# Performance work log

Measured on AMD Instinct MI355X. Metric: run time of the kernel, lower is better.

## Reference

```python
import jax, jax.numpy as jnp
import numpy as np

B, T, D, H, K, V, W = 2, 2048, 768, 12, 64, 64, 1024
EPS = 1e-6


def setup_inputs() -> dict:
    key = jax.random.key(0)
    ks = jax.random.split(key, 10)
    std = 0.02
    return {
        "x": jax.random.normal(ks[0], (B, T, D), jnp.float32),
        "gdn_state": jax.random.normal(ks[1], (B, H, K, V), jnp.float32),
        "Wq": jax.random.normal(ks[2], (D, H * K), jnp.float32) * std,
        "Wk": jax.random.normal(ks[3], (D, H * K), jnp.float32) * std,
        "Wv": jax.random.normal(ks[4], (D, H * K), jnp.float32) * std,
        "Wo": jax.random.normal(ks[5], (H * K, D), jnp.float32) * std,
        "Wgq": jax.random.normal(ks[6], (D, H * K), jnp.float32) * std,
        "Wro": jax.random.normal(ks[7], (H * V, D), jnp.float32) * std,
        "Wg": jax.random.normal(ks[8], (D, H), jnp.float32) * std,
        "bg": jnp.full((H,), 1.0, jnp.float32),  # swa_gate_init
        "norm_w": jnp.ones((D,), jnp.float32),
    }


def reference(x, gdn_state, Wq, Wk, Wv, Wo, Wgq, Wro, Wg, bg, norm_w):
    # RMSNorm
    xn = x * jax.lax.rsqrt(jnp.mean(x * x, axis=-1, keepdims=True) + EPS) * norm_w

    def proj(w):  # (B,T,D)@(D,HK) -> (B,H,T,K)
        return (xn @ w).reshape(B, T, H, K).transpose(0, 2, 1, 3)

    q, k, v = proj(Wq), proj(Wk), proj(Wv)
    scale = K ** -0.5

    scores = jnp.einsum("bhqk,bhsk->bhqs", q, k) * scale  # (B,H,T,T)
    i = jnp.arange(T)[:, None]
    j = jnp.arange(T)[None, :]
    allowed = (j <= i) & (j >= i - W)  # causal sliding window
    scores = jnp.where(allowed, scores, -jnp.inf)
    attn = jax.nn.softmax(scores, axis=-1)

    local = jnp.einsum("bhqs,bhsk->bhqk", attn, v)
    local = local.transpose(0, 2, 1, 3).reshape(B, T, H * K) @ Wo  # (B,T,D)

    # GDN state retrieval
    qg = jax.nn.relu((xn @ Wgq).reshape(B, T, H, K).transpose(0, 2, 1, 3))  # (B,H,T,K)
    retrieved = jnp.einsum("bhkv,bhtk->bhtv", gdn_state, qg)  # (B,H,T,V)
    retrieval = retrieved.transpose(0, 2, 1, 3).reshape(B, T, H * V) @ Wro  # (B,T,D)
    gate = jax.nn.sigmoid(xn @ Wg + bg)  # (B,T,H)
    retrieval = jnp.mean(gate, axis=-1, keepdims=True) * retrieval

    return x + local + retrieval
```

## Files before the change

kernel.cpp:

```cpp
#include <hip/hip_runtime.h>
#include <math.h>
#include <stdint.h>

typedef float f32x4 __attribute__((ext_vector_type(4)));
typedef __bf16 bf16x8 __attribute__((ext_vector_type(8)));
typedef __bf16 bf16x4 __attribute__((ext_vector_type(4)));

constexpr int Bc = 2, Tc = 2048, Dc = 768, Hc = 12, Wc = 1024;
#define CEXP 0.18033688011112042f

__device__ __forceinline__ f32x4 mfma_bf16(bf16x8 a, bf16x8 b, f32x4 c) {
    return __builtin_amdgcn_mfma_f32_16x16x32_bf16(a, b, c, 0, 0, 0);
}
__device__ __forceinline__ void gload16(const void* g, void* l) {
    __builtin_amdgcn_global_load_lds(
        (const __attribute__((address_space(1))) uint32_t*)g,
        (__attribute__((address_space(3))) uint32_t*)l, 16, 0, 0);
}
__device__ __forceinline__ uint32_t pack2(float a, float b) {
    union { __bf16 h[2]; uint32_t u; } x;
    x.h[0] = (__bf16)a; x.h[1] = (__bf16)b; return x.u;
}
__device__ __forceinline__ void s_wait_vm4() { asm volatile("s_waitcnt vmcnt(4)" ::: "memory"); }
__device__ __forceinline__ void s_wait_vm2() { asm volatile("s_waitcnt vmcnt(2)" ::: "memory"); }
__device__ __forceinline__ void s_wait_vm0() { asm volatile("s_waitcnt vmcnt(0)" ::: "memory"); }
__device__ __forceinline__ void s_wait_lgkm0() { asm volatile("s_waitcnt lgkmcnt(0)" ::: "memory"); }
__device__ __forceinline__ void bar()        { __builtin_amdgcn_s_barrier(); }
__device__ __forceinline__ void wait_tiles2(int infl) {
    if (infl >= 2) s_wait_vm4();
    else if (infl == 1) s_wait_vm2();
    else s_wait_vm0();
}

__global__ __launch_bounds__(256) void k_prep_w(
    const float* __restrict__ Wq, const float* __restrict__ Wk,
    const float* __restrict__ Wv, const float* __restrict__ Wgq,
    const float* __restrict__ Wo, const float* __restrict__ Wro,
    __bf16* __restrict__ wTproj, __bf16* __restrict__ wTout)
{
    __shared__ __bf16 ldsT[64][66];
    const int wsel = blockIdx.y;
    const float* srcs[6] = {Wq, Wk, Wv, Wgq, Wo, Wro};
    const float* src = srcs[wsel];
    __bf16* dst; int dstride, koff;
    if (wsel < 4) { dst = wTproj + (size_t)wsel * Dc * Dc; dstride = Dc;  koff = 0; }
    else if (wsel == 4) { dst = wTout; dstride = 1536; koff = 0; }
    else { dst = wTout; dstride = 1536; koff = 768; }
    const float scale = (wsel == 0) ? CEXP : 1.0f;

    int tile = blockIdx.x;
    int tk = tile % 12, tn = tile / 12;
    int k0 = tk * 64, n0 = tn * 64;
    int i = threadIdx.x, rsub = i >> 4, c4 = i & 15;
#pragma unroll
    for (int rep = 0; rep < 4; ++rep) {
        int row = rep * 16 + rsub;
        float4 v = *(const float4*)(src + (size_t)(k0 + row) * Dc + n0 + c4 * 4);
        ldsT[c4 * 4 + 0][row] = (__bf16)(v.x * scale);
        ldsT[c4 * 4 + 1][row] = (__bf16)(v.y * scale);
        ldsT[c4 * 4 + 2][row] = (__bf16)(v.z * scale);
        ldsT[c4 * 4 + 3][row] = (__bf16)(v.w * scale);
    }
    __syncthreads();
#pragma unroll
    for (int rep = 0; rep < 4; ++rep) {
        int n = rep * 16 + rsub;
        bf16x4 o = *(const bf16x4*)&ldsT[n][c4 * 4];
        *(bf16x4*)(dst + (size_t)(n0 + n) * dstride + koff + k0 + c4 * 4) = o;
    }
}

__global__ __launch_bounds__(256) void k_prep_state(
    const float* __restrict__ st, __bf16* __restrict__ stT)
{
    int idx = blockIdx.x * 256 + threadIdx.x;
    int bh = idx >> 12, kk = (idx >> 6) & 63, vv = idx & 63;
    stT[(size_t)bh * 4096 + vv * 64 + kk] = (__bf16)st[idx];
}

__global__ __launch_bounds__(256) void k_norm_gate(
    const float* __restrict__ x, const float* __restrict__ norm_w,
    const float* __restrict__ Wg, const float* __restrict__ bg,
    __bf16* __restrict__ xnb, float* __restrict__ gmean)
{
    int row = blockIdx.x, tid = threadIdx.x;
    int wv = tid >> 6;
    const float* xr = x + (size_t)row * Dc;
    float4 v = make_float4(0.f, 0.f, 0.f, 0.f);
    float ss = 0.f;
    if (tid < 192) {
        v = ((const float4*)xr)[tid];
        ss = v.x * v.x + v.y * v.y + v.z * v.z + v.w * v.w;
    }
#pragma unroll
    for (int m = 32; m; m >>= 1) ss += __shfl_xor(ss, m, 64);
    __shared__ float red[4];
    __shared__ float pred[4][12];
    if ((tid & 63) == 0) red[wv] = ss;
    __syncthreads();
    float tot = red[0] + red[1] + red[2] + red[3];
    float rms = rsqrtf(tot * (1.f / 768.f) + 1e-6f);
    float xn0 = 0.f, xn1 = 0.f, xn2 = 0.f, xn3 = 0.f;
    if (tid < 192) {
        float4 nw = ((const float4*)norm_w)[tid];
        xn0 = v.x * rms * nw.x; xn1 = v.y * rms * nw.y;
        xn2 = v.z * rms * nw.z; xn3 = v.w * rms * nw.w;
        bf16x4 o;
        o[0] = (__bf16)xn0; o[1] = (__bf16)xn1; o[2] = (__bf16)xn2; o[3] = (__bf16)xn3;
        *(bf16x4*)(xnb + (size_t)row * Dc + tid * 4) = o;
    }
    float p[12];
#pragma unroll
    for (int h = 0; h < 12; ++h) p[h] = 0.f;
    if (tid < 192) {
        const float* wr = Wg + (size_t)tid * 48;
#pragma unroll
        for (int h = 0; h < 12; ++h)
            p[h] = xn0 * wr[h] + xn1 * wr[12 + h] + xn2 * wr[24 + h] + xn3 * wr[36 + h];
    }
#pragma unroll
    for (int h = 0; h < 12; ++h) {
#pragma unroll
        for (int m = 32; m; m >>= 1) p[h] += __shfl_xor(p[h], m, 64);
    }
    if ((tid & 63) == 0) {
#pragma unroll
        for (int h = 0; h < 12; ++h) pred[wv][h] = p[h];
    }
    __syncthreads();
    if (tid == 0) {
        float s = 0.f;
#pragma unroll
        for (int h = 0; h < 12; ++h) {
            float ph = pred[0][h] + pred[1][h] + pred[2][h] + pred[3][h];
            s += 1.f / (1.f + expf(-(ph + bg[h])));
        }
        gmean[row] = s * (1.f / 12.f);
    }
}

template <int MODE>
__global__ __launch_bounds__(256) void k_gemm(
    const __bf16* __restrict__ A, const __bf16* __restrict__ BT,
    const float* __restrict__ xres, float* __restrict__ outf,
    __bf16* __restrict__ qb, __bf16* __restrict__ kbf,
    __bf16* __restrict__ vtb, __bf16* __restrict__ qgb)
{
    constexpr int BM = (MODE == 0) ? 128 : 64;
    constexpr int BN = (MODE == 0) ? 128 : 64;
    constexpr int KD = (MODE == 0) ? 768 : 1536;
    constexpr int BK = (MODE == 0) ? 32 : 64;
    constexpr int KI = BK / 32;
    constexpr int WM = BM / 2, WN = BN / 2;
    constexpr int MI = WM / 16, NI = WN / 16;
    constexpr int NK = KD / BK;
    constexpr int GR = BK / 8;
    constexpr int ACH = BM * BK / 2048;
    constexpr int BCH = BN * BK / 2048;
    __shared__ __bf16 As[2][BM * BK];
    __shared__ __bf16 Bs[2][BN * BK];
    const int tid = threadIdx.x, w = tid >> 6, lane = tid & 63;
    const int g = lane >> 4, t = lane & 15;
    int id = blockIdx.x, xcd = id & 7, l = id >> 3;
    int m0, n0;
    if (MODE == 0) {
        m0 = (((xcd & 3) * 8) + (l & 7)) * BM;
        n0 = (((xcd >> 2) * 12) + (l >> 3)) * BN;
    } else {
        m0 = ((xcd * 8) + (l & 7)) * BM;
        n0 = (l >> 3) * BN;
    }
    const __bf16* Abase = A + (size_t)m0 * KD;
    const __bf16* Bbase = BT + (size_t)n0 * KD;
    const int wrow = (w >> 1) * WM, wcol = (w & 1) * WN;

    auto STAGE = [&](int buf, int k0) {
#pragma unroll
        for (int c = 0; c < ACH; ++c) {
            int chunk = c * 256 + tid, row = chunk / GR, cix = chunk % GR;
            gload16(Abase + (size_t)row * KD + k0 + cix * 8, &As[buf][chunk * 8]);
        }
#pragma unroll
        for (int c = 0; c < BCH; ++c) {
            int chunk = c * 256 + tid, row = chunk / GR, cix = chunk % GR;
            gload16(Bbase + (size_t)row * KD + k0 + cix * 8, &Bs[buf][chunk * 8]);
        }
    };

    f32x4 acc[MI][NI] = {};
    STAGE(0, 0);
    STAGE(1, BK);
    for (int ks = 0; ks < NK; ++ks) {
        if (ks == NK - 1) s_wait_vm0(); else s_wait_vm4();
        bar();
        const __bf16* Ab = As[ks & 1];
        const __bf16* Bb = Bs[ks & 1];
        bf16x8 af[MI][KI], bfr[NI][KI];
#pragma unroll
        for (int kk = 0; kk < KI; ++kk) {
#pragma unroll
            for (int mi = 0; mi < MI; ++mi)
                af[mi][kk] = *(const bf16x8*)(Ab + (wrow + mi * 16 + t) * BK + kk * 32 + g * 8);
#pragma unroll
            for (int ni = 0; ni < NI; ++ni)
                bfr[ni][kk] = *(const bf16x8*)(Bb + (wcol + ni * 16 + t) * BK + kk * 32 + g * 8);
        }
        s_wait_lgkm0();
        __builtin_amdgcn_sched_barrier(0);
        bar();
        if (ks + 2 < NK) STAGE(ks & 1, (ks + 2) * BK);
        __builtin_amdgcn_s_setprio(1);
#pragma unroll
        for (int kk = 0; kk < KI; ++kk)
#pragma unroll
            for (int mi = 0; mi < MI; ++mi)
#pragma unroll
                for (int ni = 0; ni < NI; ++ni)
                    acc[mi][ni] = mfma_bf16(af[mi][kk], bfr[ni][kk], acc[mi][ni]);
        __builtin_amdgcn_s_setprio(0);
    }
    const int region = (MODE == 0) ? (n0 / 768) : 0;
    if (MODE == 0 && region == 2) {
#pragma unroll
        for (int mi = 0; mi < MI; ++mi)
#pragma unroll
            for (int ni = 0; ni < NI; ++ni) {
                int grow0 = m0 + wrow + mi * 16 + g * 4;
                int b = grow0 >> 11, ti0 = grow0 & (Tc - 1);
                int c = (n0 + wcol + ni * 16 + t) - 1536;
                int h = c >> 6, kd = c & 63;
                int kap = ti0 & 63;
                int rho = (kap & 32) | (((kap >> 2) & 3) << 3) | (((kap >> 4) & 1) << 2);
                int ts = (ti0 & ~63) | (rho ^ ((kd & 7) << 3));
                bf16x4 o;
                o[0] = (__bf16)acc[mi][ni][0]; o[1] = (__bf16)acc[mi][ni][1];
                o[2] = (__bf16)acc[mi][ni][2]; o[3] = (__bf16)acc[mi][ni][3];
                *(bf16x4*)(vtb + ((size_t)(b * Hc + h) * 64 + kd) * Tc + ts) = o;
            }
    } else {
#pragma unroll
        for (int mi = 0; mi < MI; ++mi)
#pragma unroll
            for (int ni = 0; ni < NI; ++ni)
#pragma unroll
                for (int r = 0; r < 4; ++r) {
                    int grow = m0 + wrow + mi * 16 + g * 4 + r;
                    int gcol = n0 + wcol + ni * 16 + t;
                    float v = acc[mi][ni][r];
                    if (MODE == 1) {
                        size_t idx = (size_t)grow * Dc + gcol;
                        outf[idx] = xres[idx] + v;
                    } else {
                        int c = gcol - region * 768;
                        int h = c >> 6, kd = c & 63;
                        int b = grow >> 11, ti = grow & (Tc - 1);
                        if (region == 0)
                            qb[((size_t)(b * Hc + h) * Tc + ti) * 64 + kd] = (__bf16)v;
                        else if (region == 1) {
                            int kds = kd ^ ((ti & 7) << 3);
                            kbf[((size_t)(b * Hc + h) * Tc + ti) * 64 + kds] = (__bf16)v;
                        } else
                            qgb[((size_t)(b * Hc + h) * Tc + ti) * 64 + kd] = (__bf16)fmaxf(v, 0.f);
                    }
                }
    }
}

__global__ __launch_bounds__(512, 6) void k_attn(
    const __bf16* __restrict__ q, const __bf16* __restrict__ k,
    const __bf16* __restrict__ vt, const __bf16* __restrict__ qg,
    const __bf16* __restrict__ stateT, const float* __restrict__ gmean,
    __bf16* __restrict__ ac)
{
    __shared__ __bf16 Ks[3][64 * 64];
    __shared__ __bf16 Vs[3][64 * 64];
    int id = blockIdx.x, xcd = id & 7, l = id >> 3;
    int nid = xcd * 96 + l;
    int sblk = nid & 31, h = (nid >> 5) % Hc, b = nid / (32 * Hc);
    int tid = threadIdx.x;
    int w = tid >> 6, lane = tid & 63;
    int g = lane >> 4, t = lane & 15;
    int q0 = sblk * 64, qw = q0 + (w & 3) * 16;
    const int myPar = w >> 2;
    const __bf16* qb = q + (size_t)(b * Hc + h) * Tc * 64;
    const __bf16* kb = k + (size_t)(b * Hc + h) * Tc * 64;
    const __bf16* vb = vt + (size_t)(b * Hc + h) * 64 * Tc;

    bf16x8 qf0 = *(const bf16x8*)(qb + (size_t)(qw + t) * 64 + g * 8);
    bf16x8 qf1 = *(const bf16x8*)(qb + (size_t)(qw + t) * 64 + 32 + g * 8);

    const int qi = qw + t;
    const int lowB = qi - Wc;
    const int xr = t & 7;

    f32x4 oacc[4] = {};
    float lsum = 0.f;

    const int s_begin = (q0 >= Wc) ? q0 - Wc : 0;
    const int NT = (q0 + 64 - s_begin) >> 6;

    auto STAGE = [&](int buf, int s0) {
        int ch = tid;
        gload16(kb + (size_t)(s0 + (ch >> 3)) * 64 + (ch & 7) * 8, &Ks[buf][ch * 8]);
        gload16(vb + (size_t)(ch >> 3) * Tc + s0 + (ch & 7) * 8, &Vs[buf][ch * 8]);
    };

    STAGE(0, s_begin);
    if (NT > 1) STAGE(1, s_begin + 64);
    if (NT > 2) STAGE(2, s_begin + 128);
    int buf = 0;
    for (int it = 0; it < NT; ++it) {
        int s0 = s_begin + it * 64;
        wait_tiles2(NT - 1 - it);
        bar();
        if ((it & 1) == myPar) {
            const __bf16* Kt = Ks[buf];
            const __bf16* Vt = Vs[buf];
            f32x4 sc[4];
            __builtin_amdgcn_s_setprio(1);
#pragma unroll
            for (int sub = 0; sub < 4; ++sub) {
                const __bf16* kr = Kt + (sub * 16 + t) * 64;
                bf16x8 kA = *(const bf16x8*)(kr + ((g ^ xr) << 3));
                bf16x8 kB = *(const bf16x8*)(kr + (((g + 4) ^ xr) << 3));
                f32x4 s = {};
                s = mfma_bf16(kA, qf0, s);
                s = mfma_bf16(kB, qf1, s);
                sc[sub] = s;
            }
            __builtin_amdgcn_s_setprio(0);
            float pv[4][4];
            bool fullT = (s0 + 63 <= qw) && (s0 >= qw + 15 - Wc);
            if (fullT) {
#pragma unroll
                for (int sub = 0; sub < 4; ++sub)
#pragma unroll
                    for (int r = 0; r < 4; ++r) {
                        float e = exp2f(sc[sub][r]);
                        pv[sub][r] = e;
                        lsum += e;
                    }
            } else {
#pragma unroll
                for (int sub = 0; sub < 4; ++sub)
#pragma unroll
                    for (int r = 0; r < 4; ++r) {
                        int kk = s0 + sub * 16 + g * 4 + r;
                        float e = exp2f(sc[sub][r]);
                        float val = (kk <= qi && kk >= lowB) ? e : 0.f;
                        pv[sub][r] = val;
                        lsum += val;
                    }
            }
            __builtin_amdgcn_s_setprio(1);
#pragma unroll
            for (int ks = 0; ks < 2; ++ks) {
                union { uint32_t u[4]; bf16x8 v; } pf;
                pf.u[0] = pack2(pv[ks * 2][0], pv[ks * 2][1]);
                pf.u[1] = pack2(pv[ks * 2][2], pv[ks * 2][3]);
                pf.u[2] = pack2(pv[ks * 2 + 1][0], pv[ks * 2 + 1][1]);
                pf.u[3] = pack2(pv[ks * 2 + 1][2], pv[ks * 2 + 1][3]);
#pragma unroll
                for (int n = 0; n < 4; ++n) {
                    const __bf16* vrow = Vt + (n * 16 + t) * 64;
                    bf16x8 vf = *(const bf16x8*)(vrow + ((((ks * 4) + g) ^ xr) << 3));
                    oacc[n] = mfma_bf16(pf.v, vf, oacc[n]);
                }
            }
            __builtin_amdgcn_s_setprio(0);
        }
        s_wait_lgkm0();
        __builtin_amdgcn_sched_barrier(0);
        bar();
        if (it + 3 < NT) STAGE(buf, s0 + 192);
        buf = (buf == 2) ? 0 : buf + 1;
    }
    float* cb = (float*)&Ks[0][0];
    if (w >= 4) {
        float* dst = cb + ((size_t)((w - 4) * 64 + lane)) * 20;
#pragma unroll
        for (int n = 0; n < 4; ++n) *(f32x4*)(dst + n * 4) = oacc[n];
        dst[16] = lsum;
    }
    bar();
    if (w < 4) {
        const float* src = cb + ((size_t)(w * 64 + lane)) * 20;
#pragma unroll
        for (int n = 0; n < 4; ++n) oacc[n] += *(const f32x4*)(src + n * 4);
        lsum += src[16];
        lsum += __shfl_xor(lsum, 16, 64);
        lsum += __shfl_xor(lsum, 32, 64);
        float linv = 1.f / lsum;
        float lq[4];
#pragma unroll
        for (int r = 0; r < 4; ++r) lq[r] = __shfl(linv, g * 4 + r, 64);
#pragma unroll
        for (int n = 0; n < 4; ++n)
#pragma unroll
            for (int r = 0; r < 4; ++r) {
                int qrow = qw + g * 4 + r;
                ac[(size_t)(b * Tc + qrow) * 1536 + h * 64 + n * 16 + t] =
                    (__bf16)(oacc[n][r] * lq[r]);
            }
        const __bf16* qgp = qg + (size_t)(b * Hc + h) * Tc * 64;
        const __bf16* sb = stateT + (size_t)(b * Hc + h) * 4096;
        bf16x8 a0 = *(const bf16x8*)(qgp + (size_t)(qw + t) * 64 + g * 8);
        bf16x8 a1 = *(const bf16x8*)(qgp + (size_t)(qw + t) * 64 + 32 + g * 8);
#pragma unroll
        for (int n = 0; n < 4; ++n) {
            bf16x8 b0 = *(const bf16x8*)(sb + (n * 16 + t) * 64 + g * 8);
            bf16x8 b1 = *(const bf16x8*)(sb + (n * 16 + t) * 64 + 32 + g * 8);
            f32x4 acc2 = {};
            acc2 = mfma_bf16(a0, b0, acc2);
            acc2 = mfma_bf16(a1, b1, acc2);
#pragma unroll
            for (int r = 0; r < 4; ++r) {
                int ti = qw + g * 4 + r;
                float gm = gmean[b * Tc + ti];
                ac[(size_t)(b * Tc + ti) * 1536 + 768 + h * 64 + n * 16 + t] =
                    (__bf16)(acc2[r] * gm);
            }
        }
    }
}

extern "C" void kernel_launch(void* const* d_in, const int* in_sizes, int n_in,
                              void* d_out, int out_size, void* d_ws, size_t ws_size,
                              hipStream_t stream) {
    (void)in_sizes; (void)n_in; (void)out_size; (void)ws_size;
    const float* x     = (const float*)d_in[0];
    const float* gdn   = (const float*)d_in[1];
    const float* Wq    = (const float*)d_in[2];
    const float* Wk    = (const float*)d_in[3];
    const float* Wv    = (const float*)d_in[4];
    const float* Wo    = (const float*)d_in[5];
    const float* Wgq   = (const float*)d_in[6];
    const float* Wro   = (const float*)d_in[7];
    const float* Wg    = (const float*)d_in[8];
    const float* bg    = (const float*)d_in[9];
    const float* normw = (const float*)d_in[10];
    float* out = (float*)d_out;

    char* p = (char*)d_ws;
    auto alloc = [&](size_t bytes) -> char* {
        char* r = p; p += (bytes + 255) & ~(size_t)255; return r;
    };
    constexpr size_t NROW = (size_t)Bc * Tc;
    __bf16* xnb    = (__bf16*)alloc(NROW * Dc * 2);
    __bf16* wTproj = (__bf16*)alloc((size_t)4 * Dc * Dc * 2);
    __bf16* wTout  = (__bf16*)alloc((size_t)Dc * 1536 * 2);
    __bf16* stT    = (__bf16*)alloc((size_t)Bc * Hc * 64 * 64 * 2);
    __bf16* qbuf   = (__bf16*)alloc(NROW * Dc * 2);
    __bf16* kbuf   = (__bf16*)alloc(NROW * Dc * 2);
    __bf16* qgbuf  = (__bf16*)alloc(NROW * Dc * 2);
    __bf16* vtbuf  = (__bf16*)alloc(NROW * Dc * 2);
    __bf16* ac     = (__bf16*)alloc(NROW * 1536 * 2);
    float*  gmean  = (float*)alloc(NROW * 4);

    k_prep_w<<<dim3(144, 6), 256, 0, stream>>>(Wq, Wk, Wv, Wgq, Wo, Wro, wTproj, wTout);
    k_prep_state<<<(Bc * Hc * 64 * 64) / 256, 256, 0, stream>>>(gdn, stT);
    k_norm_gate<<<NROW, 256, 0, stream>>>(x, normw, Wg, bg, xnb, gmean);

    k_gemm<0><<<768, 256, 0, stream>>>(xnb, wTproj, nullptr, nullptr,
                                       qbuf, kbuf, vtbuf, qgbuf);
    k_attn<<<768, 512, 0, stream>>>(qbuf, kbuf, vtbuf, qgbuf, stT, gmean, ac);
    k_gemm<1><<<768, 256, 0, stream>>>(ac, wTout, x, out,
                                       nullptr, nullptr, nullptr, nullptr);
}
```

Before: 114.9 us.

## Enlarge GEMM tiles to 128x384/128x96 with 512-thread blocks and split loaders

Both projection GEMMs now use 512-thread blocks with larger output tiles (128x384 for the QKV projection, 128x96 for the output projection), launching 256 blocks instead of 768. The loaders are split so one group of threads stages A and the rest stage B, with per-group vmcnt waits, and the epilogue computes the output region per 16-column fragment because a tile now spans regions. The aim is more operand reuse per LDS load and a single wave of blocks on the GPU's 256 CUs. The cost is a much larger accumulator per thread (24 MFMA tiles in mode 0), which raises register pressure, and a larger LDS footprint per block.

```diff
diff --git a/kernel.cpp b/kernel.cpp
--- a/kernel.cpp
+++ b/kernel.cpp
@@ -22,6 +22,7 @@
     x.h[0] = (__bf16)a; x.h[1] = (__bf16)b; return x.u;
 }
 __device__ __forceinline__ void s_wait_vm4() { asm volatile("s_waitcnt vmcnt(4)" ::: "memory"); }
+__device__ __forceinline__ void s_wait_vm3() { asm volatile("s_waitcnt vmcnt(3)" ::: "memory"); }
 __device__ __forceinline__ void s_wait_vm2() { asm volatile("s_waitcnt vmcnt(2)" ::: "memory"); }
 __device__ __forceinline__ void s_wait_vm0() { asm volatile("s_waitcnt vmcnt(0)" ::: "memory"); }
 __device__ __forceinline__ void s_wait_lgkm0() { asm volatile("s_waitcnt lgkmcnt(0)" ::: "memory"); }
@@ -140,23 +141,20 @@
 }
 
 template <int MODE>
-__global__ __launch_bounds__(256) void k_gemm(
+__global__ __launch_bounds__(512, 2) void k_gemm(
     const __bf16* __restrict__ A, const __bf16* __restrict__ BT,
     const float* __restrict__ xres, float* __restrict__ outf,
     __bf16* __restrict__ qb, __bf16* __restrict__ kbf,
     __bf16* __restrict__ vtb, __bf16* __restrict__ qgb)
 {
-    constexpr int BM = (MODE == 0) ? 128 : 64;
-    constexpr int BN = (MODE == 0) ? 128 : 64;
+    constexpr int BM = 128;
+    constexpr int BN = (MODE == 0) ? 384 : 96;
     constexpr int KD = (MODE == 0) ? 768 : 1536;
     constexpr int BK = (MODE == 0) ? 32 : 64;
     constexpr int KI = BK / 32;
-    constexpr int WM = BM / 2, WN = BN / 2;
-    constexpr int MI = WM / 16, NI = WN / 16;
+    constexpr int MI = 2, NI = (MODE == 0) ? 12 : 3;
     constexpr int NK = KD / BK;
-    constexpr int GR = BK / 8;
-    constexpr int ACH = BM * BK / 2048;
-    constexpr int BCH = BN * BK / 2048;
+    constexpr int WNW = (MODE == 0) ? 192 : 48;
     __shared__ __bf16 As[2][BM * BK];
     __shared__ __bf16 Bs[2][BN * BK];
     const int tid = threadIdx.x, w = tid >> 6, lane = tid & 63;
@@ -165,25 +163,47 @@
     int m0, n0;
     if (MODE == 0) {
         m0 = (((xcd & 3) * 8) + (l & 7)) * BM;
-        n0 = (((xcd >> 2) * 12) + (l >> 3)) * BN;
+        n0 = (((xcd >> 2) * 4) + (l >> 3)) * BN;
     } else {
-        m0 = ((xcd * 8) + (l & 7)) * BM;
-        n0 = (l >> 3) * BN;
+        m0 = ((xcd * 4) + (l & 3)) * BM;
+        n0 = (l >> 2) * BN;
     }
     const __bf16* Abase = A + (size_t)m0 * KD;
     const __bf16* Bbase = BT + (size_t)n0 * KD;
-    const int wrow = (w >> 1) * WM, wcol = (w & 1) * WN;
+    const int wrow = (w >> 1) * 32, wcol = (w & 1) * WNW;
+    const bool isA = (tid < 256);
 
     auto STAGE = [&](int buf, int k0) {
-#pragma unroll
-        for (int c = 0; c < ACH; ++c) {
-            int chunk = c * 256 + tid, row = chunk / GR, cix = chunk % GR;
-            gload16(Abase + (size_t)row * KD + k0 + cix * 8, &As[buf][chunk * 8]);
-        }
-#pragma unroll
-        for (int c = 0; c < BCH; ++c) {
-            int chunk = c * 256 + tid, row = chunk / GR, cix = chunk % GR;
-            gload16(Bbase + (size_t)row * KD + k0 + cix * 8, &Bs[buf][chunk * 8]);
+        if (MODE == 0) {
+            if (tid < 128) {
+#pragma unroll
+                for (int c = 0; c < 4; ++c) {
+                    int chunk = c * 128 + tid, row = chunk >> 2, cix = chunk & 3;
+                    gload16(Abase + (size_t)row * KD + k0 + cix * 8, &As[buf][chunk * 8]);
+                }
+            } else {
+                int bi = tid - 128;
+#pragma unroll
+                for (int c = 0; c < 4; ++c) {
+                    int chunk = c * 384 + bi, row = chunk >> 2, cix = chunk & 3;
+                    gload16(Bbase + (size_t)row * KD + k0 + cix * 8, &Bs[buf][chunk * 8]);
+                }
+            }
+        } else {
+            if (tid < 256) {
+#pragma unroll
+                for (int c = 0; c < 4; ++c) {
+                    int chunk = c * 256 + tid, row = chunk >> 3, cix = chunk & 7;
+                    gload16(Abase + (size_t)row * KD + k0 + cix * 8, &As[buf][chunk * 8]);
+                }
+            } else {
+                int bi = tid - 256;
+#pragma unroll
+                for (int c = 0; c < 3; ++c) {
+                    int chunk = c * 256 + bi, row = chunk >> 3, cix = chunk & 7;
+                    gload16(Bbase + (size_t)row * KD + k0 + cix * 8, &Bs[buf][chunk * 8]);
+                }
+            }
         }
     };
 
@@ -191,7 +211,10 @@
     STAGE(0, 0);
     STAGE(1, BK);
     for (int ks = 0; ks < NK; ++ks) {
-        if (ks == NK - 1) s_wait_vm0(); else s_wait_vm4();
+        if (ks == NK - 1) s_wait_vm0();
+        else if (MODE == 0) s_wait_vm4();
+        else if (isA) s_wait_vm4();
+        else s_wait_vm3();
         bar();
         const __bf16* Ab = As[ks & 1];
         const __bf16* Bb = Bs[ks & 1];
@@ -219,41 +242,42 @@
                     acc[mi][ni] = mfma_bf16(af[mi][kk], bfr[ni][kk], acc[mi][ni]);
         __builtin_amdgcn_s_setprio(0);
     }
-    const int region = (MODE == 0) ? (n0 / 768) : 0;
-    if (MODE == 0 && region == 2) {
-#pragma unroll
-        for (int mi = 0; mi < MI; ++mi)
-#pragma unroll
-            for (int ni = 0; ni < NI; ++ni) {
-                int grow0 = m0 + wrow + mi * 16 + g * 4;
-                int b = grow0 >> 11, ti0 = grow0 & (Tc - 1);
-                int c = (n0 + wcol + ni * 16 + t) - 1536;
-                int h = c >> 6, kd = c & 63;
-                int kap = ti0 & 63;
-                int rho = (kap & 32) | (((kap >> 2) & 3) << 3) | (((kap >> 4) & 1) << 2);
-                int ts = (ti0 & ~63) | (rho ^ ((kd & 7) << 3));
-                bf16x4 o;
-                o[0] = (__bf16)acc[mi][ni][0]; o[1] = (__bf16)acc[mi][ni][1];
-                o[2] = (__bf16)acc[mi][ni][2]; o[3] = (__bf16)acc[mi][ni][3];
-                *(bf16x4*)(vtb + ((size_t)(b * Hc + h) * 64 + kd) * Tc + ts) = o;
-            }
-    } else {
-#pragma unroll
-        for (int mi = 0; mi < MI; ++mi)
-#pragma unroll
-            for (int ni = 0; ni < NI; ++ni)
+#pragma unroll
+    for (int mi = 0; mi < MI; ++mi)
+#pragma unroll
+        for (int ni = 0; ni < NI; ++ni) {
+            if (MODE == 1) {
 #pragma unroll
                 for (int r = 0; r < 4; ++r) {
                     int grow = m0 + wrow + mi * 16 + g * 4 + r;
                     int gcol = n0 + wcol + ni * 16 + t;
-                    float v = acc[mi][ni][r];
-                    if (MODE == 1) {
-                        size_t idx = (size_t)grow * Dc + gcol;
-                        outf[idx] = xres[idx] + v;
-                    } else {
-                        int c = gcol - region * 768;
+                    size_t idx = (size_t)grow * Dc + gcol;
+                    outf[idx] = xres[idx] + acc[mi][ni][r];
+                }
+            } else {
+                int coln = n0 + wcol + ni * 16;
+                int region = coln / 768;
+                int cb = coln - region * 768;
+                if (region == 2) {
+                    int grow0 = m0 + wrow + mi * 16 + g * 4;
+                    int b = grow0 >> 11, ti0 = grow0 & (Tc - 1);
+                    int c = cb + t;
+                    int h = c >> 6, kd = c & 63;
+                    int kap = ti0 & 63;
+                    int rho = (kap & 32) | (((kap >> 2) & 3) << 3) | (((kap >> 4) & 1) << 2);
+                    int ts = (ti0 & ~63) | (rho ^ ((kd & 7) << 3));
+                    bf16x4 o;
+                    o[0] = (__bf16)acc[mi][ni][0]; o[1] = (__bf16)acc[mi][ni][1];
+                    o[2] = (__bf16)acc[mi][ni][2]; o[3] = (__bf16)acc[mi][ni][3];
+                    *(bf16x4*)(vtb + ((size_t)(b * Hc + h) * 64 + kd) * Tc + ts) = o;
+                } else {
+#pragma unroll
+                    for (int r = 0; r < 4; ++r) {
+                        int grow = m0 + wrow + mi * 16 + g * 4 + r;
+                        int b = grow >> 11, ti = grow & (Tc - 1);
+                        int c = cb + t;
                         int h = c >> 6, kd = c & 63;
-                        int b = grow >> 11, ti = grow & (Tc - 1);
+                        float v = acc[mi][ni][r];
                         if (region == 0)
                             qb[((size_t)(b * Hc + h) * Tc + ti) * 64 + kd] = (__bf16)v;
                         else if (region == 1) {
@@ -263,7 +287,8 @@
                             qgb[((size_t)(b * Hc + h) * Tc + ti) * 64 + kd] = (__bf16)fmaxf(v, 0.f);
                     }
                 }
-    }
+            }
+        }
 }
 
 __global__ __launch_bounds__(512, 6) void k_attn(
@@ -461,9 +486,9 @@
     k_prep_state<<<(Bc * Hc * 64 * 64) / 256, 256, 0, stream>>>(gdn, stT);
     k_norm_gate<<<NROW, 256, 0, stream>>>(x, normw, Wg, bg, xnb, gmean);
 
-    k_gemm<0><<<768, 256, 0, stream>>>(xnb, wTproj, nullptr, nullptr,
+    k_gemm<0><<<256, 512, 0, stream>>>(xnb, wTproj, nullptr, nullptr,
                                        qbuf, kbuf, vtbuf, qgbuf);
     k_attn<<<768, 512, 0, stream>>>(qbuf, kbuf, vtbuf, qgbuf, stT, gmean, ac);
-    k_gemm<1><<<768, 256, 0, stream>>>(ac, wTout, x, out,
+    k_gemm<1><<<256, 512, 0, stream>>>(ac, wTout, x, out,
                                        nullptr, nullptr, nullptr, nullptr);
 }
```

Result: slower. 131.2 us (+14.1%).
